# Kernel optimization log

Hardware: AMD Instinct MI355X
Metric: run time of the kernel (lower is better)

## Reference

```python
import jax, jax.numpy as jnp
import numpy as np

B, W, C, N = 16, 512, 4096, 8  # batch, words, coordinates, heads; k = C//N == W required by module math


def setup_inputs() -> dict:
    key = jax.random.key(0)
    ks = jax.random.split(key, 6)
    return {
        "x": jax.random.normal(ks[0], (B, W, C), dtype=jnp.float32),
        "W1": jax.random.normal(ks[1], (C, C), dtype=jnp.float32) * 0.02,
        "b1": jax.random.normal(ks[2], (C,), dtype=jnp.float32) * 0.02,
        "pre_metric": jax.random.normal(ks[3], (N, W, W), dtype=jnp.float32) * 0.02,
        "W2": jax.random.normal(ks[4], (C, C), dtype=jnp.float32) * 0.02,
        "b2": jax.random.normal(ks[5], (C,), dtype=jnp.float32) * 0.02,
    }


def reference(x, W1, b1, pre_metric, W2, b2):
    b, w, c = x.shape
    n = pre_metric.shape[0]
    k = c // n  # == w by construction
    tril = jnp.tril(jnp.ones((w, w), dtype=x.dtype))
    # causal-masked lower-triangular factor, metric M = L L^T per head
    L = pre_metric * tril                         # (n, w, w)
    M = jnp.einsum('nuv,nwv->nuw', L, L)          # (n, w, w)
    # single shared projection
    P = (x @ W1.T + b1).reshape(b, w, n, k).transpose(0, 2, 1, 3)  # (b, n, w, k)
    # bilinear quadratic form scores: P^T M P  -> (b, n, k, k) with k == w
    MP = jnp.einsum('nuv,bnvj->bnuj', M, P)       # (b, n, w, k)
    S = jnp.einsum('bnui,bnuj->bnij', P, MP)      # (b, n, k, k)
    S = S / jnp.sqrt(jnp.asarray(k, x.dtype))
    # causal zero-fill (no softmax)
    S = S * tril
    out = jnp.einsum('bnij,bnjk->bnik', S, P)     # (b, n, w, k)
    out = out.transpose(0, 2, 1, 3).reshape(b, w, c)
    return out @ W2.T + b2
```

## Files before the change

### kernel.cpp

```cpp
#include <hip/hip_runtime.h>
#include <stdint.h>

typedef uint16_t u16;
typedef short short8 __attribute__((ext_vector_type(8)));
typedef float f32x4 __attribute__((ext_vector_type(4)));

__device__ __forceinline__ u16 f2bf(float f){
  uint32_t u = __float_as_uint(f);
  u += 0x7fff + ((u >> 16) & 1);
  return (u16)(u >> 16);
}

__device__ __forceinline__ void gload_lds16(const u16* g, const char* l){
  __builtin_amdgcn_global_load_lds((const __attribute__((address_space(1))) void*)g,
                                   (__attribute__((address_space(3))) void*)l,
                                   16, 0, 0);
}

__global__ void cast_bf16_kernel(const float* __restrict__ src, u16* __restrict__ dst, long n8){
  long i = (long)blockIdx.x * blockDim.x + threadIdx.x;
  long stride = (long)gridDim.x * blockDim.x;
  for (; i < n8; i += stride){
    float4 a = *(const float4*)(src + i*8);
    float4 b = *(const float4*)(src + i*8 + 4);
    u16 r[8] = {f2bf(a.x), f2bf(a.y), f2bf(a.z), f2bf(a.w),
                f2bf(b.x), f2bf(b.y), f2bf(b.z), f2bf(b.w)};
    *(uint4*)(dst + i*8) = *(const uint4*)r;
  }
}

__global__ void mask_cast_L_kernel(const float* __restrict__ pre, u16* __restrict__ L){
  long i = (long)blockIdx.x * blockDim.x + threadIdx.x;
  if (i >= 8L*512*64) return;
  int v0 = (int)(i & 63) * 8;
  int u  = (int)((i >> 6) & 511);
  float4 a = *(const float4*)(pre + i*8);
  float4 b = *(const float4*)(pre + i*8 + 4);
  float vals[8] = {a.x,a.y,a.z,a.w,b.x,b.y,b.z,b.w};
  u16 r[8];
  #pragma unroll
  for (int j=0;j<8;j++) r[j] = f2bf((v0 + j <= u) ? vals[j] : 0.0f);
  *(uint4*)(L + i*8) = *(const uint4*)r;
}

template<int EPI, bool SWZ>
__global__ __launch_bounds__(512, 1)
void gemmp(const u16* __restrict__ A, const u16* __restrict__ B,
           void* __restrict__ Cv, int K, int lda, int ldb, int ldc,
           long asb, long asn, long bsb, long bsn, long csb, long csn,
           const float* __restrict__ bias, float scale, int tri)
{
  extern __shared__ __align__(16) char smem[];
  const int t = threadIdx.x;
  const int lane = t & 63;
  const int wave = t >> 6;
  const int wm = wave >> 2;
  const int wn = wave & 3;
  const long zb = blockIdx.z >> 3, zn = blockIdx.z & 7;
  A += zb*asb + zn*asn;
  B += zb*bsb + zn*bsn;

  int bx = blockIdx.x, by = blockIdx.y;
  if constexpr (SWZ){
    int nbx = gridDim.x;
    int bid = bx + by * nbx;
    int chunk = (nbx * gridDim.y) >> 3;
    int b2 = (bid & 7) * chunk + (bid >> 3);
    bx = b2 % nbx;  by = b2 / nbx;
  }
  const int row0 = by * 256, col0 = bx * 256;
  const int l15 = lane & 15, l4 = lane >> 4;

  const int srow = t >> 2;
  const int scol = (((t & 3) ^ ((srow >> 1) & 3)) * 8);
  const u16* gA = A + (long)(row0 + srow)*lda + scol;
  const u16* gB = B + (long)(col0 + srow)*ldb + scol;
  const long a128 = 128L*(long)lda, b128 = 128L*(long)ldb;
  const int ldst = t * 16;

  const int csw = (l4 ^ ((l15 >> 1) & 3)) * 16;
  const int raw = (wm*128 + l15)*64 + csw;
  const int rbw = 16384 + (wn*64 + l15)*64 + csw;

  f32x4 acc[8][4];
  #pragma unroll
  for (int m=0;m<8;m++)
    #pragma unroll
    for (int n=0;n<4;n++) acc[m][n] = (f32x4){0.f,0.f,0.f,0.f};

  int Keff = K;
  if (tri == 2) Keff = (row0 + 256 < K) ? (row0 + 256) : K;
  const int NT = Keff >> 5;
  const bool skipall = (tri == 1) && (col0 >= row0 + 256);

  if (!skipall){
    short8 bfS[2][4], af1S[2][4], af2[4];

#define STAGEM(PA, PB, BUF) { \
  gload_lds16((PA),        smem + (BUF)*32768 +         ldst); \
  gload_lds16((PA) + a128, smem + (BUF)*32768 +  8192 + ldst); \
  gload_lds16((PB),        smem + (BUF)*32768 + 16384 + ldst); \
  gload_lds16((PB) + b128, smem + (BUF)*32768 + 24576 + ldst); }

#define BODY(CUR, NXT, P, Q, DOST, PA, PB, VMS) { \
  const char* bn_ = smem + (NXT)*32768; \
  _Pragma("unroll") \
  for (int n=0;n<4;n++) bfS[Q][n] = *(const short8*)(bn_ + rbw + n*1024); \
  _Pragma("unroll") \
  for (int m=0;m<4;m++) af1S[Q][m] = *(const short8*)(bn_ + raw + m*1024); \
  if (DOST) STAGEM(PA, PB, ((CUR)+3)&3) \
  __builtin_amdgcn_sched_barrier(0); \
  __builtin_amdgcn_s_setprio(1); \
  _Pragma("unroll") \
  for (int m=0;m<4;m++) \
    _Pragma("unroll") \
    for (int n=0;n<4;n++) \
      acc[m][n] = __builtin_amdgcn_mfma_f32_16x16x32_bf16(af1S[P][m], bfS[P][n], acc[m][n],0,0,0); \
  _Pragma("unroll") \
  for (int m=0;m<4;m++) \
    _Pragma("unroll") \
    for (int n=0;n<4;n++) \
      acc[m+4][n] = __builtin_amdgcn_mfma_f32_16x16x32_bf16(af2[m], bfS[P][n], acc[m+4][n],0,0,0); \
  __builtin_amdgcn_s_setprio(0); \
  __builtin_amdgcn_sched_barrier(0); \
  _Pragma("unroll") \
  for (int m=0;m<4;m++) af2[m] = *(const short8*)(bn_ + raw + (m+4)*1024); \
  asm volatile("s_waitcnt vmcnt(" VMS ")" ::: "memory"); \
  __builtin_amdgcn_s_barrier(); \
  asm volatile("" ::: "memory"); }

    STAGEM(gA,      gB,      0)
    STAGEM(gA + 32, gB + 32, 1)
    STAGEM(gA + 64, gB + 64, 2)
    asm volatile("s_waitcnt vmcnt(4)" ::: "memory");
    __builtin_amdgcn_s_barrier();
    asm volatile("" ::: "memory");
    {
      const char* b0_ = smem;
      #pragma unroll
      for (int n=0;n<4;n++) bfS[0][n]  = *(const short8*)(b0_ + rbw + n*1024);
      #pragma unroll
      for (int m=0;m<4;m++) af1S[0][m] = *(const short8*)(b0_ + raw + m*1024);
      #pragma unroll
      for (int m=0;m<4;m++) af2[m]     = *(const short8*)(b0_ + raw + (m+4)*1024);
    }

    #pragma unroll 1
    for (int tb = 0; tb < NT - 4; tb += 4){
      const u16* pa = gA + (long)(tb + 3)*32;
      const u16* pb = gB + (long)(tb + 3)*32;
      BODY(0, 1, 0, 1, true, pa,      pb,      "4")
      BODY(1, 2, 1, 0, true, pa + 32, pb + 32, "4")
      BODY(2, 3, 0, 1, true, pa + 64, pb + 64, "4")
      BODY(3, 0, 1, 0, true, pa + 96, pb + 96, "4")
    }
    {
      const u16* pa = gA + (long)(NT - 1)*32;
      const u16* pb = gB + (long)(NT - 1)*32;
      BODY(0, 1, 0, 1, true,  pa, pb, "4")
      BODY(1, 2, 1, 0, false, pa, pb, "0")
      BODY(2, 3, 0, 1, false, pa, pb, "0")
      BODY(3, 0, 1, 0, false, pa, pb, "0")
    }
#undef STAGEM
#undef BODY
  }

  if constexpr (EPI == 3){
    float* C = (float*)Cv;
    #pragma unroll
    for (int m=0;m<8;m++){
      int r0 = row0 + wm*128 + m*16 + l4*4;
      #pragma unroll
      for (int n=0;n<4;n++){
        int c = col0 + wn*64 + n*16 + l15;
        float bc = bias[c];
        #pragma unroll
        for (int g=0; g<4; g++)
          C[(long)(r0+g)*ldc + c] = acc[m][n][g] + bc;
      }
    }
  } else {
    u16* C = (u16*)Cv + zb*csb + zn*csn;
    #pragma unroll
    for (int m=0;m<8;m++){
      int r0 = row0 + wm*128 + m*16 + l4*4;
      #pragma unroll
      for (int n=0;n<4;n++){
        int c = col0 + wn*64 + n*16 + l15;
        #pragma unroll
        for (int g=0;g<4;g++){
          float v = acc[m][n][g];
          int r = r0 + g;
          if constexpr (EPI==1) v += bias[r];
          if constexpr (EPI==2) v = (c <= r) ? v*scale : 0.0f;
          C[(long)r*ldc + c] = f2bf(v);
        }
      }
    }
  }
}


#define LDSB 131072

extern "C" void kernel_launch(void* const* d_in, const int* in_sizes, int n_in,
                              void* d_out, int out_size, void* d_ws, size_t ws_size,
                              hipStream_t stream)
{
  (void)in_sizes; (void)n_in; (void)out_size; (void)ws_size;
  const float* x   = (const float*)d_in[0];
  const float* W1  = (const float*)d_in[1];
  const float* b1  = (const float*)d_in[2];
  const float* pre = (const float*)d_in[3];
  const float* W2  = (const float*)d_in[4];
  const float* b2  = (const float*)d_in[5];
  float* out = (float*)d_out;
  char* ws = (char*)d_ws;

  u16* xb  = (u16*)(ws + 0L);
  u16* W1b = (u16*)(ws + 67108864L);
  u16* W2b = (u16*)(ws + 100663296L);
  u16* Lb  = (u16*)(ws + 134217728L);
  u16* Mb  = (u16*)(ws + 138412032L);
  u16* Pt  = (u16*)(ws + 142606336L);
  u16* MPt = (u16*)(ws + 209715200L);
  u16* Sb  = (u16*)(ws + 276824064L);
  u16* Ob  = MPt;

  hipFuncSetAttribute((const void*)gemmp<0,false>, hipFuncAttributeMaxDynamicSharedMemorySize, LDSB);
  hipFuncSetAttribute((const void*)gemmp<1,true >, hipFuncAttributeMaxDynamicSharedMemorySize, LDSB);
  hipFuncSetAttribute((const void*)gemmp<2,false>, hipFuncAttributeMaxDynamicSharedMemorySize, LDSB);
  hipFuncSetAttribute((const void*)gemmp<3,true >, hipFuncAttributeMaxDynamicSharedMemorySize, LDSB);

  cast_bf16_kernel<<<4096,256,0,stream>>>(x,  xb,  4194304L);
  cast_bf16_kernel<<<4096,256,0,stream>>>(W1, W1b, 2097152L);
  cast_bf16_kernel<<<4096,256,0,stream>>>(W2, W2b, 2097152L);
  mask_cast_L_kernel<<<1024,256,0,stream>>>(pre, Lb);

  gemmp<0,false><<<dim3(2,2,8),512,LDSB,stream>>>(Lb, Lb, Mb, 512, 512,512,512,
      0, 262144, 0, 262144, 0, 262144, nullptr, 0.f, 0);

  gemmp<1,true><<<dim3(32,16,1),512,LDSB,stream>>>(W1b, xb, Pt, 4096, 4096,4096,8192,
      0,0, 0,0, 0,0, b1, 0.f, 0);

  gemmp<0,false><<<dim3(2,2,128),512,LDSB,stream>>>(Pt, Mb, MPt, 512, 8192,512,512,
      512, 512L*8192, 0, 262144, 8L*262144, 262144, nullptr, 0.f, 0);

  gemmp<2,false><<<dim3(2,2,128),512,LDSB,stream>>>(Pt, MPt, Sb, 512, 8192,512,512,
      512, 512L*8192, 8L*262144, 262144, 8L*262144, 262144, nullptr, 0.04419417382f, 1);

  gemmp<0,false><<<dim3(2,2,128),512,LDSB,stream>>>(Sb, Pt, Ob, 512, 512,8192,4096,
      8L*262144, 262144, 512, 512L*8192, 512L*4096, 512, nullptr, 0.f, 2);

  gemmp<3,true><<<dim3(16,32,1),512,LDSB,stream>>>(Ob, W2b, out, 4096, 4096,4096,4096,
      0,0, 0,0, 0,0, b2, 0.f, 0);
}
```

Baseline: 825.6 us.

## Rewrite GEMM with 4 waves and 32x32x16 MFMA tiles, swizzle all launches

Replaces the 8-wave GEMM, built on 16x16x32 MFMA, with a 4-wave version where each wave computes a 128x128 sub-tile using 32x32x16 bf16 MFMAs. LDS fragment reads are split into two K-halves and double-buffered across the two MFMA groups. Global-to-LDS staging now takes 8 loads per thread. The block-ID swizzle is extended over the z dimension and turned on for every launch. This aims for higher MFMA efficiency and fewer LDS reads per FLOP, at the cost of fewer waves to hide latency and more accumulator registers per thread.

Measured after the change: 834.7 us. No clear change (+1.1%).

```diff
diff --git a/kernel.cpp b/kernel.cpp
--- a/kernel.cpp
+++ b/kernel.cpp
@@ -3,7 +3,7 @@
 
 typedef uint16_t u16;
 typedef short short8 __attribute__((ext_vector_type(8)));
-typedef float f32x4 __attribute__((ext_vector_type(4)));
+typedef float f32x16 __attribute__((ext_vector_type(16)));
 
 __device__ __forceinline__ u16 f2bf(float f){
   uint32_t u = __float_as_uint(f);
@@ -44,49 +44,51 @@
 }
 
 template<int EPI, bool SWZ>
-__global__ __launch_bounds__(512, 1)
-void gemmp(const u16* __restrict__ A, const u16* __restrict__ B,
-           void* __restrict__ Cv, int K, int lda, int ldb, int ldc,
-           long asb, long asn, long bsb, long bsn, long csb, long csn,
-           const float* __restrict__ bias, float scale, int tri)
+__global__ __launch_bounds__(256, 1)
+void gemm4w(const u16* __restrict__ A, const u16* __restrict__ B,
+            void* __restrict__ Cv, int K, int lda, int ldb, int ldc,
+            long asb, long asn, long bsb, long bsn, long csb, long csn,
+            const float* __restrict__ bias, float scale, int tri)
 {
   extern __shared__ __align__(16) char smem[];
   const int t = threadIdx.x;
   const int lane = t & 63;
   const int wave = t >> 6;
-  const int wm = wave >> 2;
-  const int wn = wave & 3;
-  const long zb = blockIdx.z >> 3, zn = blockIdx.z & 7;
+  const int wm = wave >> 1;
+  const int wn = wave & 1;
+
+  int bx = blockIdx.x, by = blockIdx.y, bz = blockIdx.z;
+  if constexpr (SWZ){
+    int nbx = gridDim.x, nxy = gridDim.x * gridDim.y;
+    int bid = bx + by*nbx + bz*nxy;
+    int chunk = (nxy * gridDim.z) >> 3;
+    int b2 = (bid & 7) * chunk + (bid >> 3);
+    bz = b2 / nxy; int rem = b2 - bz*nxy;
+    by = rem / nbx; bx = rem - by*nbx;
+  }
+  const long zb = bz >> 3, zn = bz & 7;
   A += zb*asb + zn*asn;
   B += zb*bsb + zn*bsn;
-
-  int bx = blockIdx.x, by = blockIdx.y;
-  if constexpr (SWZ){
-    int nbx = gridDim.x;
-    int bid = bx + by * nbx;
-    int chunk = (nbx * gridDim.y) >> 3;
-    int b2 = (bid & 7) * chunk + (bid >> 3);
-    bx = b2 % nbx;  by = b2 / nbx;
-  }
   const int row0 = by * 256, col0 = bx * 256;
-  const int l15 = lane & 15, l4 = lane >> 4;
+  const int lr = lane & 31, hi = lane >> 5;
 
   const int srow = t >> 2;
-  const int scol = (((t & 3) ^ ((srow >> 1) & 3)) * 8);
+  const int scol = (((t & 3) ^ ((t >> 2) & 3)) * 8);
   const u16* gA = A + (long)(row0 + srow)*lda + scol;
   const u16* gB = B + (long)(col0 + srow)*ldb + scol;
-  const long a128 = 128L*(long)lda, b128 = 128L*(long)ldb;
-  const int ldst = t * 16;
-
-  const int csw = (l4 ^ ((l15 >> 1) & 3)) * 16;
-  const int raw = (wm*128 + l15)*64 + csw;
-  const int rbw = 16384 + (wn*64 + l15)*64 + csw;
-
-  f32x4 acc[8][4];
+  const long a64 = 64L*(long)lda, b64 = 64L*(long)ldb;
+  const int t16 = t * 16;
+
+  const int sw  = (hi ^ (lr & 3)) * 16;
+  const int aof0 = (wm*128 + lr)*64 + sw;          const int aof1 = aof0 ^ 32;
+  const int bof0 = 16384 + (wn*128 + lr)*64 + sw;  const int bof1 = bof0 ^ 32;
+
+  f32x16 acc[4][4];
   #pragma unroll
-  for (int m=0;m<8;m++)
+  for (int mb=0;mb<4;mb++)
     #pragma unroll
-    for (int n=0;n<4;n++) acc[m][n] = (f32x4){0.f,0.f,0.f,0.f};
+    for (int nb=0;nb<4;nb++)
+      acc[mb][nb] = (f32x16)(0.f);
 
   int Keff = K;
   if (tri == 2) Keff = (row0 + 256 < K) ? (row0 + 256) : K;
@@ -94,104 +96,103 @@
   const bool skipall = (tri == 1) && (col0 >= row0 + 256);
 
   if (!skipall){
-    short8 bfS[2][4], af1S[2][4], af2[4];
+    short8 afA[4], bfA[4], afB[4], bfB[4];
 
 #define STAGEM(PA, PB, BUF) { \
-  gload_lds16((PA),        smem + (BUF)*32768 +         ldst); \
-  gload_lds16((PA) + a128, smem + (BUF)*32768 +  8192 + ldst); \
-  gload_lds16((PB),        smem + (BUF)*32768 + 16384 + ldst); \
-  gload_lds16((PB) + b128, smem + (BUF)*32768 + 24576 + ldst); }
-
-#define BODY(CUR, NXT, P, Q, DOST, PA, PB, VMS) { \
-  const char* bn_ = smem + (NXT)*32768; \
-  _Pragma("unroll") \
-  for (int n=0;n<4;n++) bfS[Q][n] = *(const short8*)(bn_ + rbw + n*1024); \
-  _Pragma("unroll") \
-  for (int m=0;m<4;m++) af1S[Q][m] = *(const short8*)(bn_ + raw + m*1024); \
-  if (DOST) STAGEM(PA, PB, ((CUR)+3)&3) \
+  const u16* pa_ = (PA); const u16* pb_ = (PB); \
+  gload_lds16(pa_,          smem + (BUF)*32768 +         t16); \
+  gload_lds16(pa_ +   a64,  smem + (BUF)*32768 +  4096 + t16); \
+  gload_lds16(pa_ + 2*a64,  smem + (BUF)*32768 +  8192 + t16); \
+  gload_lds16(pa_ + 3*a64,  smem + (BUF)*32768 + 12288 + t16); \
+  gload_lds16(pb_,          smem + (BUF)*32768 + 16384 + t16); \
+  gload_lds16(pb_ +   b64,  smem + (BUF)*32768 + 20480 + t16); \
+  gload_lds16(pb_ + 2*b64,  smem + (BUF)*32768 + 24576 + t16); \
+  gload_lds16(pb_ + 3*b64,  smem + (BUF)*32768 + 28672 + t16); }
+
+#define RD_A(D) { \
+  _Pragma("unroll") for (int mb=0;mb<4;mb++) afA[mb] = *(const short8*)(smem + (D)*32768 + aof0 + mb*2048); \
+  _Pragma("unroll") for (int nb=0;nb<4;nb++) bfA[nb] = *(const short8*)(smem + (D)*32768 + bof0 + nb*2048); }
+#define RD_B(D) { \
+  _Pragma("unroll") for (int mb=0;mb<4;mb++) afB[mb] = *(const short8*)(smem + (D)*32768 + aof1 + mb*2048); \
+  _Pragma("unroll") for (int nb=0;nb<4;nb++) bfB[nb] = *(const short8*)(smem + (D)*32768 + bof1 + nb*2048); }
+#define MMA(AF, BF) { \
+  _Pragma("unroll") for (int mb=0;mb<4;mb++) \
+  _Pragma("unroll") for (int nb=0;nb<4;nb++) \
+    acc[mb][nb] = __builtin_amdgcn_mfma_f32_32x32x16_bf16(AF[mb], BF[nb], acc[mb][nb], 0, 0, 0); }
+
+#define BODY(D, DOST, PA, PB, VM) { \
+  RD_B(D); \
   __builtin_amdgcn_sched_barrier(0); \
-  __builtin_amdgcn_s_setprio(1); \
-  _Pragma("unroll") \
-  for (int m=0;m<4;m++) \
-    _Pragma("unroll") \
-    for (int n=0;n<4;n++) \
-      acc[m][n] = __builtin_amdgcn_mfma_f32_16x16x32_bf16(af1S[P][m], bfS[P][n], acc[m][n],0,0,0); \
-  _Pragma("unroll") \
-  for (int m=0;m<4;m++) \
-    _Pragma("unroll") \
-    for (int n=0;n<4;n++) \
-      acc[m+4][n] = __builtin_amdgcn_mfma_f32_16x16x32_bf16(af2[m], bfS[P][n], acc[m+4][n],0,0,0); \
-  __builtin_amdgcn_s_setprio(0); \
+  MMA(afA, bfA); \
   __builtin_amdgcn_sched_barrier(0); \
-  _Pragma("unroll") \
-  for (int m=0;m<4;m++) af2[m] = *(const short8*)(bn_ + raw + (m+4)*1024); \
-  asm volatile("s_waitcnt vmcnt(" VMS ")" ::: "memory"); \
+  RD_A(((D)+1)&3); \
+  if (DOST) STAGEM(PA, PB, ((D)+3)&3) \
+  __builtin_amdgcn_sched_barrier(0); \
+  MMA(afB, bfB); \
+  asm volatile("s_waitcnt vmcnt(" VM ")" ::: "memory"); \
   __builtin_amdgcn_s_barrier(); \
   asm volatile("" ::: "memory"); }
 
     STAGEM(gA,      gB,      0)
     STAGEM(gA + 32, gB + 32, 1)
     STAGEM(gA + 64, gB + 64, 2)
-    asm volatile("s_waitcnt vmcnt(4)" ::: "memory");
+    asm volatile("s_waitcnt vmcnt(8)" ::: "memory");
     __builtin_amdgcn_s_barrier();
     asm volatile("" ::: "memory");
-    {
-      const char* b0_ = smem;
-      #pragma unroll
-      for (int n=0;n<4;n++) bfS[0][n]  = *(const short8*)(b0_ + rbw + n*1024);
-      #pragma unroll
-      for (int m=0;m<4;m++) af1S[0][m] = *(const short8*)(b0_ + raw + m*1024);
-      #pragma unroll
-      for (int m=0;m<4;m++) af2[m]     = *(const short8*)(b0_ + raw + (m+4)*1024);
-    }
+    RD_A(0)
 
     #pragma unroll 1
     for (int tb = 0; tb < NT - 4; tb += 4){
       const u16* pa = gA + (long)(tb + 3)*32;
       const u16* pb = gB + (long)(tb + 3)*32;
-      BODY(0, 1, 0, 1, true, pa,      pb,      "4")
-      BODY(1, 2, 1, 0, true, pa + 32, pb + 32, "4")
-      BODY(2, 3, 0, 1, true, pa + 64, pb + 64, "4")
-      BODY(3, 0, 1, 0, true, pa + 96, pb + 96, "4")
+      BODY(0, true, pa,      pb,      "8")
+      BODY(1, true, pa + 32, pb + 32, "8")
+      BODY(2, true, pa + 64, pb + 64, "8")
+      BODY(3, true, pa + 96, pb + 96, "8")
     }
     {
       const u16* pa = gA + (long)(NT - 1)*32;
       const u16* pb = gB + (long)(NT - 1)*32;
-      BODY(0, 1, 0, 1, true,  pa, pb, "4")
-      BODY(1, 2, 1, 0, false, pa, pb, "0")
-      BODY(2, 3, 0, 1, false, pa, pb, "0")
-      BODY(3, 0, 1, 0, false, pa, pb, "0")
+      BODY(0, true,  pa, pb, "8")
+      BODY(1, false, pa, pb, "0")
+      BODY(2, false, pa, pb, "0")
+      BODY(3, false, pa, pb, "0")
     }
 #undef STAGEM
+#undef RD_A
+#undef RD_B
+#undef MMA
 #undef BODY
   }
 
   if constexpr (EPI == 3){
     float* C = (float*)Cv;
     #pragma unroll
-    for (int m=0;m<8;m++){
-      int r0 = row0 + wm*128 + m*16 + l4*4;
+    for (int mb=0;mb<4;mb++){
+      int rb = row0 + wm*128 + mb*32 + 4*hi;
       #pragma unroll
-      for (int n=0;n<4;n++){
-        int c = col0 + wn*64 + n*16 + l15;
+      for (int nb=0;nb<4;nb++){
+        int c = col0 + wn*128 + nb*32 + lr;
         float bc = bias[c];
         #pragma unroll
-        for (int g=0; g<4; g++)
-          C[(long)(r0+g)*ldc + c] = acc[m][n][g] + bc;
+        for (int reg=0; reg<16; reg++){
+          int r = rb + (reg & 3) + 8*(reg >> 2);
+          C[(long)r*ldc + c] = acc[mb][nb][reg] + bc;
+        }
       }
     }
   } else {
     u16* C = (u16*)Cv + zb*csb + zn*csn;
     #pragma unroll
-    for (int m=0;m<8;m++){
-      int r0 = row0 + wm*128 + m*16 + l4*4;
+    for (int mb=0;mb<4;mb++){
+      int rb = row0 + wm*128 + mb*32 + 4*hi;
       #pragma unroll
-      for (int n=0;n<4;n++){
-        int c = col0 + wn*64 + n*16 + l15;
+      for (int nb=0;nb<4;nb++){
+        int c = col0 + wn*128 + nb*32 + lr;
         #pragma unroll
-        for (int g=0;g<4;g++){
-          float v = acc[m][n][g];
-          int r = r0 + g;
+        for (int reg=0; reg<16; reg++){
+          int r = rb + (reg & 3) + 8*(reg >> 2);
+          float v = acc[mb][nb][reg];
           if constexpr (EPI==1) v += bias[r];
           if constexpr (EPI==2) v = (c <= r) ? v*scale : 0.0f;
           C[(long)r*ldc + c] = f2bf(v);
@@ -228,31 +229,31 @@
   u16* Sb  = (u16*)(ws + 276824064L);
   u16* Ob  = MPt;
 
-  hipFuncSetAttribute((const void*)gemmp<0,false>, hipFuncAttributeMaxDynamicSharedMemorySize, LDSB);
-  hipFuncSetAttribute((const void*)gemmp<1,true >, hipFuncAttributeMaxDynamicSharedMemorySize, LDSB);
-  hipFuncSetAttribute((const void*)gemmp<2,false>, hipFuncAttributeMaxDynamicSharedMemorySize, LDSB);
-  hipFuncSetAttribute((const void*)gemmp<3,true >, hipFuncAttributeMaxDynamicSharedMemorySize, LDSB);
+  hipFuncSetAttribute((const void*)gemm4w<0,true>, hipFuncAttributeMaxDynamicSharedMemorySize, LDSB);
+  hipFuncSetAttribute((const void*)gemm4w<1,true>, hipFuncAttributeMaxDynamicSharedMemorySize, LDSB);
+  hipFuncSetAttribute((const void*)gemm4w<2,true>, hipFuncAttributeMaxDynamicSharedMemorySize, LDSB);
+  hipFuncSetAttribute((const void*)gemm4w<3,true>, hipFuncAttributeMaxDynamicSharedMemorySize, LDSB);
 
   cast_bf16_kernel<<<4096,256,0,stream>>>(x,  xb,  4194304L);
   cast_bf16_kernel<<<4096,256,0,stream>>>(W1, W1b, 2097152L);
   cast_bf16_kernel<<<4096,256,0,stream>>>(W2, W2b, 2097152L);
   mask_cast_L_kernel<<<1024,256,0,stream>>>(pre, Lb);
 
-  gemmp<0,false><<<dim3(2,2,8),512,LDSB,stream>>>(Lb, Lb, Mb, 512, 512,512,512,
+  gemm4w<0,true><<<dim3(2,2,8),256,LDSB,stream>>>(Lb, Lb, Mb, 512, 512,512,512,
       0, 262144, 0, 262144, 0, 262144, nullptr, 0.f, 0);
 
-  gemmp<1,true><<<dim3(32,16,1),512,LDSB,stream>>>(W1b, xb, Pt, 4096, 4096,4096,8192,
+  gemm4w<1,true><<<dim3(32,16,1),256,LDSB,stream>>>(W1b, xb, Pt, 4096, 4096,4096,8192,
       0,0, 0,0, 0,0, b1, 0.f, 0);
 
-  gemmp<0,false><<<dim3(2,2,128),512,LDSB,stream>>>(Pt, Mb, MPt, 512, 8192,512,512,
+  gemm4w<0,true><<<dim3(2,2,128),256,LDSB,stream>>>(Pt, Mb, MPt, 512, 8192,512,512,
       512, 512L*8192, 0, 262144, 8L*262144, 262144, nullptr, 0.f, 0);
 
-  gemmp<2,false><<<dim3(2,2,128),512,LDSB,stream>>>(Pt, MPt, Sb, 512, 8192,512,512,
+  gemm4w<2,true><<<dim3(2,2,128),256,LDSB,stream>>>(Pt, MPt, Sb, 512, 8192,512,512,
       512, 512L*8192, 8L*262144, 262144, 8L*262144, 262144, nullptr, 0.04419417382f, 1);
 
-  gemmp<0,false><<<dim3(2,2,128),512,LDSB,stream>>>(Sb, Pt, Ob, 512, 512,8192,4096,
+  gemm4w<0,true><<<dim3(2,2,128),256,LDSB,stream>>>(Sb, Pt, Ob, 512, 512,8192,4096,
       8L*262144, 262144, 512, 512L*8192, 512L*4096, 512, nullptr, 0.f, 2);
 
-  gemmp<3,true><<<dim3(16,32,1),512,LDSB,stream>>>(Ob, W2b, out, 4096, 4096,4096,4096,
+  gemm4w<3,true><<<dim3(16,32,1),256,LDSB,stream>>>(Ob, W2b, out, 4096, 4096,4096,4096,
       0,0, 0,0, 0,0, b2, 0.f, 0);
 }
```
